# Kernel optimization log

Measured on AMD Instinct MI355X. Metric: run time of the kernel, lower is better.

The kernel has to match this reference:

```python
import jax, jax.numpy as jnp
import numpy as np

N_NODES = 50000
N_EDGES = 400000
FEAT = 64      # irreps_in modeled as 64 scalar channels; head_dim == FEAT
HEADS = 4


def setup_inputs() -> dict:
    key = jax.random.key(0)
    k = jax.random.split(key, 7)
    x = jax.random.normal(k[0], (N_NODES, FEAT), dtype=jnp.float32)
    edge_index = jax.random.randint(k[1], (2, N_EDGES), 0, N_NODES, dtype=jnp.int32)
    s = 1.0 / np.sqrt(FEAT)
    Wq = jax.random.normal(k[2], (HEADS, FEAT, FEAT), dtype=jnp.float32) * s
    Wk = jax.random.normal(k[3], (HEADS, FEAT, FEAT), dtype=jnp.float32) * s
    Wv = jax.random.normal(k[4], (HEADS, FEAT, FEAT), dtype=jnp.float32) * s
    Wout = jax.random.normal(k[5], (FEAT, FEAT), dtype=jnp.float32) * s
    return {"x": x, "Wq": Wq, "Wk": Wk, "Wv": Wv, "Wout": Wout, "edge_index": edge_index}


def reference(x, Wq, Wk, Wv, Wout, edge_index):
    # Per-node attention over graph neighbors. The torch module pads neighbors
    # into degree buckets and runs SDPA per bucket; mathematically this is a
    # segment (per-receiver) softmax over incoming edges, which we compute
    # directly without padding or bucket loops.
    sender, receiver = edge_index[0], edge_index[1]
    n = x.shape[0]
    scale = x.shape[1] ** -0.5  # head_dim == FEAT in the original module

    Q = jnp.einsum('nf,hfd->hnd', x, Wq)  # (H, N, F)
    K = jnp.einsum('nf,hfd->hnd', x, Wk)
    V = jnp.einsum('nf,hfd->hnd', x, Wv)

    # Edge scores: q_receiver . k_sender per head -> (E, H)
    s = jnp.einsum('hef,hef->eh', Q[:, receiver], K[:, sender]) * scale

    # Numerically stable segment softmax over each receiver's neighborhood.
    m = jax.ops.segment_max(s, receiver, num_segments=n)          # (N, H)
    p = jnp.exp(s - m[receiver])                                   # (E, H)
    denom = jax.ops.segment_sum(p, receiver, num_segments=n)      # (N, H)
    alpha = p / denom[receiver]                                    # (E, H)

    # Weighted message aggregation: (H, E, F) scattered to (H, N, F).
    msg = alpha.T[:, :, None] * V[:, sender]
    agg = jax.vmap(lambda mh: jax.ops.segment_sum(mh, receiver, num_segments=n))(msg)

    out = jnp.nan_to_num(agg.mean(axis=0))  # deg-0 nodes contribute zeros
    return x + out @ Wout
```

## Files before the change

kernel.cpp:

```cpp
#include <hip/hip_runtime.h>

#define FEAT 64
#define HEADS 4
#define CAP 64
#define LROW 520
#define TSTR 80

typedef __attribute__((ext_vector_type(8))) short short8;
typedef __attribute__((ext_vector_type(8))) __bf16 bf16x8;
typedef __attribute__((ext_vector_type(4))) float floatx4;
typedef __attribute__((ext_vector_type(2))) float float2v;
typedef unsigned short ushortT;

static __device__ __forceinline__ unsigned short f2bf(float f) {
    union { float f; unsigned int u; } v; v.f = f;
    unsigned int u = v.u;
    u = u + 0x7fffu + ((u >> 16) & 1u);
    return (unsigned short)(u >> 16);
}
static __device__ __forceinline__ float bfl(unsigned int u) {
    union { unsigned int u; float f; } v; v.u = u << 16; return v.f;
}
static __device__ __forceinline__ float bfh(unsigned int u) {
    union { unsigned int u; float f; } v; v.u = u & 0xffff0000u; return v.f;
}

__global__ __launch_bounds__(256) void k_init(const float* __restrict__ Wq,
        const float* __restrict__ Wk, const float* __restrict__ Wv,
        const float* __restrict__ Wout, short8* __restrict__ Wpack,
        short8* __restrict__ WoutPack, int4* __restrict__ deg4, int nslots) {
    int t = blockIdx.x * 256 + threadIdx.x;
    if (t < nslots) deg4[t] = make_int4(0, 0, 0, 0);
    int o = t;
    if (o < 12 * 2 * 4 * 64) {
        int lane = o & 63, dt = (o >> 6) & 3, kb = (o >> 8) & 1, m = o >> 9;
        int mat = m >> 2, h = m & 3;
        const float* src = (mat == 0) ? Wq : (mat == 1) ? Wk : Wv;
        src += (size_t)h * 64 * 64;
        int d = dt * 16 + (lane & 15);
        int kbase = kb * 32 + (lane >> 4) * 8;
        short8 val;
#pragma unroll
        for (int j = 0; j < 8; j++)
            val[j] = (short)f2bf(src[(kbase + j) * 64 + d]);
        Wpack[o] = val;
    } else if (o < 6144 + 512) {
        int idx = o - 6144;
        int lane = idx & 63, kb = (idx >> 6) & 1, nt = idx >> 7;
        int d = nt * 16 + (lane & 15);
        int kbase = kb * 32 + (lane >> 4) * 8;
        short8 val;
#pragma unroll
        for (int j = 0; j < 8; j++)
            val[j] = (short)f2bf(Wout[(kbase + j) * 64 + d]);
        WoutPack[idx] = val;
    }
}

__global__ __launch_bounds__(256) void k_qkv(const float* __restrict__ x,
        const short8* __restrict__ Wpack, const int* __restrict__ send,
        const int* __restrict__ recv, int* __restrict__ deg,
        int* __restrict__ srt, ushortT* __restrict__ Qb, ushortT* __restrict__ KVb,
        int E) {
    __shared__ ushortT lds[16 * LROW];
    int e = blockIdx.x * 256 + threadIdx.x;
    if (e < E) {
        int r = recv[e];
        int pos = atomicAdd(&deg[r], 1);
        if (pos < CAP) srt[(size_t)r * CAP + pos] = send[e];
    }

    int w = threadIdx.x >> 6, lane = threadIdx.x & 63;
    int quad = lane >> 4, lrow = lane & 15;
    int ntile = blockIdx.x * 16;
    const float* xrow = x + (size_t)(ntile + lrow) * 64 + quad * 8;
    float4 fa = *(const float4*)(xrow);
    float4 fb = *(const float4*)(xrow + 4);
    float4 fc = *(const float4*)(xrow + 32);
    float4 fd = *(const float4*)(xrow + 36);
    short8 a0 = {(short)f2bf(fa.x), (short)f2bf(fa.y), (short)f2bf(fa.z), (short)f2bf(fa.w),
                 (short)f2bf(fb.x), (short)f2bf(fb.y), (short)f2bf(fb.z), (short)f2bf(fb.w)};
    short8 a1 = {(short)f2bf(fc.x), (short)f2bf(fc.y), (short)f2bf(fc.z), (short)f2bf(fc.w),
                 (short)f2bf(fd.x), (short)f2bf(fd.y), (short)f2bf(fd.z), (short)f2bf(fd.w)};
    bf16x8 X0 = __builtin_bit_cast(bf16x8, a0);
    bf16x8 X1 = __builtin_bit_cast(bf16x8, a1);
#pragma unroll
    for (int mat = 0; mat < 3; mat++) {
        int m = mat * 4 + w;
#pragma unroll
        for (int dt = 0; dt < 4; dt++) {
            floatx4 acc = {0.f, 0.f, 0.f, 0.f};
            short8 b0 = Wpack[((m * 2 + 0) * 4 + dt) * 64 + lane];
            short8 b1 = Wpack[((m * 2 + 1) * 4 + dt) * 64 + lane];
            acc = __builtin_amdgcn_mfma_f32_16x16x32_bf16(
                __builtin_bit_cast(bf16x8, b0), X0, acc, 0, 0, 0);
            acc = __builtin_amdgcn_mfma_f32_16x16x32_bf16(
                __builtin_bit_cast(bf16x8, b1), X1, acc, 0, 0, 0);
            if (mat == 0) {
                unsigned int u01 = (unsigned)f2bf(acc[0] * 0.125f)
                                 | ((unsigned)f2bf(acc[1] * 0.125f) << 16);
                unsigned int u23 = (unsigned)f2bf(acc[2] * 0.125f)
                                 | ((unsigned)f2bf(acc[3] * 0.125f) << 16);
                *(uint2*)&lds[lrow * LROW + w * 64 + dt * 16 + quad * 4]
                    = make_uint2(u01, u23);
            } else {
                int p = __builtin_amdgcn_cvt_pk_fp8_f32(acc[0], acc[1], 0, false);
                p = __builtin_amdgcn_cvt_pk_fp8_f32(acc[2], acc[3], p, true);
                int slot = w * 16 + dt * 4 + quad;
                *(unsigned int*)&lds[lrow * LROW + 256 + slot * 4 + ((mat == 2) ? 2 : 0)]
                    = (unsigned int)p;
            }
        }
    }
    __syncthreads();
    {
        int u = threadIdx.x;
#pragma unroll
        for (int rep = 0; rep < 2; rep++, u += 256) {
            int row = u >> 5, idx = u & 31;
            uint4 val = *(const uint4*)&lds[row * LROW + idx * 8];
            *(uint4*)(Qb + ((size_t)(ntile + row)) * 256 + idx * 8) = val;
        }
    }
    {
        uint4* KVq = (uint4*)KVb;
        int u = threadIdx.x;
#pragma unroll
        for (int rep = 0; rep < 2; rep++, u += 256) {
            int row = u >> 5, idx = u & 31;
            uint4 val = *(const uint4*)&lds[row * LROW + 256 + idx * 8];
            KVq[(size_t)(ntile + row) * 32 + idx] = val;
        }
    }
}

__global__ __launch_bounds__(256) void k_attn(const ushortT* __restrict__ Qb,
        const ushortT* __restrict__ KVb, const short8* __restrict__ WoutPack,
        const int* __restrict__ deg, const int* __restrict__ srt,
        const float* __restrict__ x, float* __restrict__ out, int N) {
    __shared__ ushortT tl[16 * TSTR];
    int w = threadIdx.x >> 6, lane = threadIdx.x & 63;
    int el = lane & 31, e_sel = lane >> 5, jj = lane & 7;
    int rb = blockIdx.x * 16;
    const uint4* KV4 = (const uint4*)KVb;

    for (int rr = 0; rr < 4; rr++) {
        int ridx = w * 4 + rr;
        int r = rb + ridx;
        uint4 qu = ((const uint4*)(Qb + (size_t)r * 256))[el];
        float q0 = bfl(qu.x), q1 = bfh(qu.x), q2 = bfl(qu.y), q3 = bfh(qu.y);
        float q4 = bfl(qu.z), q5 = bfh(qu.z), q6 = bfl(qu.w), q7 = bfh(qu.w);
        float a0 = 0.f, a1 = 0.f, a2 = 0.f, a3 = 0.f;
        float a4 = 0.f, a5 = 0.f, a6 = 0.f, a7 = 0.f, den = 0.f;
        const int* myslots = srt + (size_t)r * CAP;
        int d = min(deg[r], CAP);

#define PROC2(kv, pmask)                                                  \
    {                                                                     \
        float2v kA = __builtin_amdgcn_cvt_pk_f32_fp8(kv.x, false);        \
        float2v kB = __builtin_amdgcn_cvt_pk_f32_fp8(kv.x, true);         \
        float2v kC = __builtin_amdgcn_cvt_pk_f32_fp8(kv.z, false);        \
        float2v kD = __builtin_amdgcn_cvt_pk_f32_fp8(kv.z, true);         \
        float sp = q0 * kA.x + q1 * kA.y + q2 * kB.x + q3 * kB.y          \
                 + q4 * kC.x + q5 * kC.y + q6 * kD.x + q7 * kD.y;         \
        sp += __shfl_xor(sp, 1);                                          \
        sp += __shfl_xor(sp, 2);                                          \
        sp += __shfl_xor(sp, 4);                                          \
        float p = __expf(sp);                                             \
        p = (pmask) ? p : 0.f;                                            \
        float2v vA = __builtin_amdgcn_cvt_pk_f32_fp8(kv.y, false);        \
        float2v vB = __builtin_amdgcn_cvt_pk_f32_fp8(kv.y, true);         \
        float2v vC = __builtin_amdgcn_cvt_pk_f32_fp8(kv.w, false);        \
        float2v vD = __builtin_amdgcn_cvt_pk_f32_fp8(kv.w, true);         \
        den += p;                                                         \
        a0 += p * vA.x; a1 += p * vA.y; a2 += p * vB.x; a3 += p * vB.y;   \
        a4 += p * vC.x; a5 += p * vC.y; a6 += p * vD.x; a7 += p * vD.y;   \
    }
        int i = 0;
        for (; i + 3 < d; i += 4) {
            int4 s4 = *(const int4*)(myslots + i);
            int s01 = e_sel ? s4.y : s4.x;
            int s23 = e_sel ? s4.w : s4.z;
            uint4 kv0 = KV4[(size_t)s01 * 32 + el];
            uint4 kv1 = KV4[(size_t)s23 * 32 + el];
            PROC2(kv0, true) PROC2(kv1, true)
        }
        for (; i < d; i += 2) {
            int idx = i + e_sel;
            int slot = myslots[min(idx, d - 1)];
            uint4 kv = KV4[(size_t)slot * 32 + el];
            PROC2(kv, idx < d)
        }
#undef PROC2
        den += __shfl_xor(den, 32);
        a0 += __shfl_xor(a0, 32); a1 += __shfl_xor(a1, 32);
        a2 += __shfl_xor(a2, 32); a3 += __shfl_xor(a3, 32);
        a4 += __shfl_xor(a4, 32); a5 += __shfl_xor(a5, 32);
        a6 += __shfl_xor(a6, 32); a7 += __shfl_xor(a7, 32);
        float inv = (den > 0.f) ? 0.25f / den : 0.f;
        a0 *= inv; a1 *= inv; a2 *= inv; a3 *= inv;
        a4 *= inv; a5 *= inv; a6 *= inv; a7 *= inv;
        a0 += __shfl_xor(a0, 8);  a1 += __shfl_xor(a1, 8);
        a2 += __shfl_xor(a2, 8);  a3 += __shfl_xor(a3, 8);
        a4 += __shfl_xor(a4, 8);  a5 += __shfl_xor(a5, 8);
        a6 += __shfl_xor(a6, 8);  a7 += __shfl_xor(a7, 8);
        a0 += __shfl_xor(a0, 16); a1 += __shfl_xor(a1, 16);
        a2 += __shfl_xor(a2, 16); a3 += __shfl_xor(a3, 16);
        a4 += __shfl_xor(a4, 16); a5 += __shfl_xor(a5, 16);
        a6 += __shfl_xor(a6, 16); a7 += __shfl_xor(a7, 16);
        if (lane < 8) {
            uint4 tv;
            tv.x = (unsigned)f2bf(a0) | ((unsigned)f2bf(a1) << 16);
            tv.y = (unsigned)f2bf(a2) | ((unsigned)f2bf(a3) << 16);
            tv.z = (unsigned)f2bf(a4) | ((unsigned)f2bf(a5) << 16);
            tv.w = (unsigned)f2bf(a6) | ((unsigned)f2bf(a7) << 16);
            *(uint4*)&tl[ridx * TSTR + jj * 8] = tv;
        }
    }
    __syncthreads();

    int q = lane >> 4, c = lane & 15;
    short8 ta0 = *(const short8*)&tl[c * TSTR + q * 8];
    short8 ta1 = *(const short8*)&tl[c * TSTR + 32 + q * 8];
    short8 tb0 = WoutPack[(w * 2 + 0) * 64 + lane];
    short8 tb1 = WoutPack[(w * 2 + 1) * 64 + lane];
    floatx4 acc = {0.f, 0.f, 0.f, 0.f};
    acc = __builtin_amdgcn_mfma_f32_16x16x32_bf16(
        __builtin_bit_cast(bf16x8, ta0), __builtin_bit_cast(bf16x8, tb0), acc, 0, 0, 0);
    acc = __builtin_amdgcn_mfma_f32_16x16x32_bf16(
        __builtin_bit_cast(bf16x8, ta1), __builtin_bit_cast(bf16x8, tb1), acc, 0, 0, 0);
#pragma unroll
    for (int reg = 0; reg < 4; reg++) {
        size_t idx = (size_t)(rb + q * 4 + reg) * 64 + w * 16 + c;
        out[idx] = x[idx] + acc[reg];
    }
}

extern "C" void kernel_launch(void* const* d_in, const int* in_sizes, int n_in,
                              void* d_out, int out_size, void* d_ws, size_t ws_size,
                              hipStream_t stream) {
    const float* x    = (const float*)d_in[0];
    const float* Wq   = (const float*)d_in[1];
    const float* Wk   = (const float*)d_in[2];
    const float* Wv   = (const float*)d_in[3];
    const float* Wout = (const float*)d_in[4];
    const int*   ei   = (const int*)d_in[5];
    int N = in_sizes[0] / FEAT;
    int E = in_sizes[5] / 2;
    const int* send = ei;
    const int* recv = ei + E;

    char* ws = (char*)d_ws;
    size_t o = 0;
    auto alloc = [&](size_t bytes) {
        void* p = ws + o;
        o = (o + bytes + 255) & ~(size_t)255;
        return p;
    };
    ushortT* Qb      = (ushortT*)alloc((size_t)N * 256 * 2);
    ushortT* KVb     = (ushortT*)alloc((size_t)N * 512);
    short8* Wpack    = (short8*)alloc(6144 * sizeof(short8));
    short8* WoutPack = (short8*)alloc(512 * sizeof(short8));
    int* deg         = (int*)alloc((size_t)((N + 3) & ~3) * 4);
    int* srt         = (int*)alloc((size_t)N * CAP * 4);

    int nslots = ((N + 3) & ~3) / 4;
    k_init<<<64, 256, 0, stream>>>(Wq, Wk, Wv, Wout, Wpack, WoutPack,
                                   (int4*)deg, nslots);
    k_qkv<<<N / 16, 256, 0, stream>>>(x, Wpack, send, recv, deg, srt, Qb, KVb, E);
    k_attn<<<N / 16, 256, 0, stream>>>(Qb, KVb, WoutPack, deg, srt, x,
                                       (float*)d_out, N);
}
```

Baseline: 156.9 us.

## Bucket edges by receiver range using per-block LDS histograms instead of global atomics

Moves edge bucketing out of the QKV projection kernel into a prep kernel. There, 64 blocks each own a contiguous range of receivers, scan the whole receiver array, and count degrees with shared-memory atomics before writing the degrees out. This removes the global atomics and the deg zeroing, but every bucketing block must read the full edge list, and the work now runs on only 64 blocks before the projection starts.

```diff
diff --git a/kernel.cpp b/kernel.cpp
--- a/kernel.cpp
+++ b/kernel.cpp
@@ -5,6 +5,8 @@
 #define CAP 64
 #define LROW 520
 #define TSTR 80
+#define SCB 64
+#define RPB 782
 
 typedef __attribute__((ext_vector_type(8))) short short8;
 typedef __attribute__((ext_vector_type(8))) __bf16 bf16x8;
@@ -25,51 +27,66 @@
     union { unsigned int u; float f; } v; v.u = u & 0xffff0000u; return v.f;
 }
 
-__global__ __launch_bounds__(256) void k_init(const float* __restrict__ Wq,
+__global__ __launch_bounds__(256) void k_prep(const float* __restrict__ Wq,
         const float* __restrict__ Wk, const float* __restrict__ Wv,
         const float* __restrict__ Wout, short8* __restrict__ Wpack,
-        short8* __restrict__ WoutPack, int4* __restrict__ deg4, int nslots) {
-    int t = blockIdx.x * 256 + threadIdx.x;
-    if (t < nslots) deg4[t] = make_int4(0, 0, 0, 0);
-    int o = t;
-    if (o < 12 * 2 * 4 * 64) {
-        int lane = o & 63, dt = (o >> 6) & 3, kb = (o >> 8) & 1, m = o >> 9;
-        int mat = m >> 2, h = m & 3;
-        const float* src = (mat == 0) ? Wq : (mat == 1) ? Wk : Wv;
-        src += (size_t)h * 64 * 64;
-        int d = dt * 16 + (lane & 15);
-        int kbase = kb * 32 + (lane >> 4) * 8;
-        short8 val;
-#pragma unroll
-        for (int j = 0; j < 8; j++)
-            val[j] = (short)f2bf(src[(kbase + j) * 64 + d]);
-        Wpack[o] = val;
-    } else if (o < 6144 + 512) {
-        int idx = o - 6144;
-        int lane = idx & 63, kb = (idx >> 6) & 1, nt = idx >> 7;
-        int d = nt * 16 + (lane & 15);
-        int kbase = kb * 32 + (lane >> 4) * 8;
-        short8 val;
-#pragma unroll
-        for (int j = 0; j < 8; j++)
-            val[j] = (short)f2bf(Wout[(kbase + j) * 64 + d]);
-        WoutPack[idx] = val;
+        short8* __restrict__ WoutPack, const int* __restrict__ send,
+        const int* __restrict__ recv, int* __restrict__ deg,
+        int* __restrict__ srt, int N, int E) {
+    int b = blockIdx.x, t = threadIdx.x;
+    if (b < SCB) {
+        __shared__ int hist[RPB];
+        for (int i = t; i < RPB; i += 256) hist[i] = 0;
+        __syncthreads();
+        int lo = b * RPB;
+        int hi = min(lo + RPB, N);
+        const int4* recv4 = (const int4*)recv;
+        int n4 = E >> 2;
+        for (int i4 = t; i4 < n4; i4 += 256) {
+            int4 rv = recv4[i4];
+            int e = i4 * 4;
+#define TRY(rr, ee)                                                       \
+            if ((rr) >= lo && (rr) < hi) {                                \
+                int pos = atomicAdd(&hist[(rr) - lo], 1);                 \
+                if (pos < CAP) srt[(size_t)(rr) * CAP + pos] = send[ee];  \
+            }
+            TRY(rv.x, e) TRY(rv.y, e + 1) TRY(rv.z, e + 2) TRY(rv.w, e + 3)
+#undef TRY
+        }
+        __syncthreads();
+        for (int i = t; i < hi - lo; i += 256) deg[lo + i] = hist[i];
+    } else {
+        int o = (b - SCB) * 256 + t;
+        if (o < 12 * 2 * 4 * 64) {
+            int lane = o & 63, dt = (o >> 6) & 3, kb = (o >> 8) & 1, m = o >> 9;
+            int mat = m >> 2, h = m & 3;
+            const float* src = (mat == 0) ? Wq : (mat == 1) ? Wk : Wv;
+            src += (size_t)h * 64 * 64;
+            int d = dt * 16 + (lane & 15);
+            int kbase = kb * 32 + (lane >> 4) * 8;
+            short8 val;
+#pragma unroll
+            for (int j = 0; j < 8; j++)
+                val[j] = (short)f2bf(src[(kbase + j) * 64 + d]);
+            Wpack[o] = val;
+        } else if (o < 6144 + 512) {
+            int idx = o - 6144;
+            int lane = idx & 63, kb = (idx >> 6) & 1, nt = idx >> 7;
+            int d = nt * 16 + (lane & 15);
+            int kbase = kb * 32 + (lane >> 4) * 8;
+            short8 val;
+#pragma unroll
+            for (int j = 0; j < 8; j++)
+                val[j] = (short)f2bf(Wout[(kbase + j) * 64 + d]);
+            WoutPack[idx] = val;
+        }
     }
 }
 
 __global__ __launch_bounds__(256) void k_qkv(const float* __restrict__ x,
-        const short8* __restrict__ Wpack, const int* __restrict__ send,
-        const int* __restrict__ recv, int* __restrict__ deg,
-        int* __restrict__ srt, ushortT* __restrict__ Qb, ushortT* __restrict__ KVb,
-        int E) {
+        const short8* __restrict__ Wpack, ushortT* __restrict__ Qb,
+        ushortT* __restrict__ KVb) {
     __shared__ ushortT lds[16 * LROW];
-    int e = blockIdx.x * 256 + threadIdx.x;
-    if (e < E) {
-        int r = recv[e];
-        int pos = atomicAdd(&deg[r], 1);
-        if (pos < CAP) srt[(size_t)r * CAP + pos] = send[e];
-    }
-
     int w = threadIdx.x >> 6, lane = threadIdx.x & 63;
     int quad = lane >> 4, lrow = lane & 15;
     int ntile = blockIdx.x * 16;
@@ -264,10 +281,9 @@
     int* deg         = (int*)alloc((size_t)((N + 3) & ~3) * 4);
     int* srt         = (int*)alloc((size_t)N * CAP * 4);
 
-    int nslots = ((N + 3) & ~3) / 4;
-    k_init<<<64, 256, 0, stream>>>(Wq, Wk, Wv, Wout, Wpack, WoutPack,
-                                   (int4*)deg, nslots);
-    k_qkv<<<N / 16, 256, 0, stream>>>(x, Wpack, send, recv, deg, srt, Qb, KVb, E);
+    k_prep<<<SCB + 26, 256, 0, stream>>>(Wq, Wk, Wv, Wout, Wpack, WoutPack,
+                                         send, recv, deg, srt, N, E);
+    k_qkv<<<N / 16, 256, 0, stream>>>(x, Wpack, Qb, KVb);
     k_attn<<<N / 16, 256, 0, stream>>>(Qb, KVb, WoutPack, deg, srt, x,
                                        (float*)d_out, N);
 }
```

After: 460.8 us. 2.94x slower.
